# Kernel tuning notes

Hardware: AMD Instinct MI355X
Metric: run time of the kernel (lower is better)

The kernel has to match this reference:

```python
import jax, jax.numpy as jnp
import numpy as np

B, C, H, W = 4, 256, 128, 128
HEADS = 64
HD = C // HEADS  # 4
G = 32           # group norm groups
EPS = 1e-5


def setup_inputs() -> dict:
    key = jax.random.key(0)
    ks = jax.random.split(key, 6)
    x = jax.random.normal(ks[0], (B, C, H, W), dtype=jnp.float32)
    gn_weight = jnp.ones((1, C, 1, 1), dtype=jnp.float32)
    gn_bias = jnp.zeros((1, C, 1, 1), dtype=jnp.float32)
    # 1x1 convs stored as (out_ch, in_ch) matrices
    qkv_w = jax.random.normal(ks[1], (3 * C, C), dtype=jnp.float32) * 0.02
    qkv_b = jax.random.normal(ks[2], (3 * C,), dtype=jnp.float32) * 0.01
    out_w = jax.random.normal(ks[3], (C, C), dtype=jnp.float32) * 0.02
    out_b = jax.random.normal(ks[4], (C,), dtype=jnp.float32) * 0.01
    return {"x": x, "gn_weight": gn_weight, "gn_bias": gn_bias,
            "qkv_w": qkv_w, "qkv_b": qkv_b, "out_w": out_w, "out_b": out_b}


def group_norm(x, weight, bias):
    n, c, h, w = x.shape
    xg = x.reshape(n, G, -1)
    mean = xg.mean(axis=-1, keepdims=True)
    var = jnp.var(xg, axis=-1, keepdims=True, ddof=1)  # torch.var default is unbiased
    xg = (xg - mean) / jnp.sqrt(var + EPS)
    return xg.reshape(n, c, h, w) * weight + bias


def conv1x1(x, w, b):
    # x: (B, Cin, H, W), w: (Cout, Cin)
    return jnp.einsum('bchw,oc->bohw', x, w) + b[None, :, None, None]


def reference(x, gn_weight, gn_bias, qkv_w, qkv_b, out_w, out_b):
    skip = x
    h = group_norm(x, gn_weight, gn_bias)
    qkv = conv1x1(h, qkv_w, qkv_b)                      # (B, 3C, H, W)
    qkv = qkv.reshape(B, HEADS, 3 * HD, H * W)
    q, k, v = jnp.split(qkv, 3, axis=2)                  # each (B, heads, hd, HW)
    scores = jnp.einsum('bhdn,bhen->bhde', q, k) / (HD ** 0.5)  # (B, heads, hd, hd)
    scores = jax.nn.softmax(scores, axis=1)              # softmax over HEADS axis (as in source)
    out = jnp.einsum('bhde,bhen->bhdn', scores, v)       # (B, heads, hd, HW)
    out = out.reshape(B, C, H, W)
    out = conv1x1(out, out_w, out_b)
    return out + skip
```

## Files before the change

kernel.cpp:

```cpp
#include <hip/hip_runtime.h>


constexpr int kB = 4;
constexpr int kC = 256;
constexpr int kHW = 16384;
constexpr int kHeads = 64;
constexpr int kNG = 32;
constexpr int kCPG = 8;
constexpr int kCP1 = 257;
constexpr int kPS = 260;
constexpr float kEPS = 1e-5f;
constexpr int kNSplit = 32;

typedef __attribute__((ext_vector_type(8))) _Float16 f16x8;
typedef __attribute__((ext_vector_type(4))) _Float16 f16x4;
typedef __attribute__((ext_vector_type(4))) float f32x4;

union V8 { f16x8 v; uint4 u; _Float16 h[8]; };

constexpr size_t oXT    = 0;
constexpr size_t oXH    = oXT + (size_t)kB * kHW * kC / 2;
constexpr size_t oSpart = oXH + (size_t)kB * kHW * kC / 2;
constexpr size_t oS     = oSpart + (size_t)3 * kB * kNSplit * 128 * 128;
constexpr size_t oSums  = oS + (size_t)kB * kCP1 * kPS;
constexpr size_t oGv    = oSums + (size_t)kB * kC;
constexpr size_t oSc    = oGv + (size_t)kB * kC;
constexpr size_t oTc    = oSc + (size_t)kB * kC;
constexpr size_t oScore = oTc + (size_t)kB * kC;
constexpr size_t oAq    = oSpart;
constexpr size_t oM     = oXH;
constexpr size_t oGmH   = oXH + (size_t)kB * kC * kPS;

__global__ __launch_bounds__(256) void k0_tr(const float* __restrict__ x,
                                             _Float16* __restrict__ xT,
                                             _Float16* __restrict__ xH,
                                             float* __restrict__ sums) {
  const int nt = blockIdx.x, ct = blockIdx.y, b = blockIdx.z;
  __shared__ float T[64][65];
  __shared__ float psum[64][4];
  const float* xb = x + ((size_t)b * kC + ct * 64) * kHW + nt * 64;
  _Float16* xhb = xH + ((size_t)b * kC + ct * 64) * kHW + nt * 64;
  const int tid = threadIdx.x;

#pragma unroll
  for (int rep = 0; rep < 4; ++rep) {
    const int r = rep * 16 + (tid >> 4);
    const int c4 = (tid & 15) * 4;
    float4 v = *(const float4*)(xb + (size_t)r * kHW + c4);
    T[r][c4 + 0] = v.x; T[r][c4 + 1] = v.y; T[r][c4 + 2] = v.z; T[r][c4 + 3] = v.w;
    f16x4 hv = {(_Float16)v.x, (_Float16)v.y, (_Float16)v.z, (_Float16)v.w};
    *(f16x4*)(xhb + (size_t)r * kHW + c4) = hv;
  }
  __syncthreads();
  {
    const int q = tid >> 6, r = tid & 63;
    float s = 0.f;
#pragma unroll
    for (int i = 0; i < 16; ++i) s += T[r][q * 16 + i];
    psum[r][q] = s;
  }
  __syncthreads();
  if (tid < 64) {
    float s = psum[tid][0] + psum[tid][1] + psum[tid][2] + psum[tid][3];
    atomicAdd(&sums[b * kC + ct * 64 + tid], s);
  }
  const int nl = tid >> 2, cgrp = tid & 3;
  V8 lo, hi;
#pragma unroll
  for (int i = 0; i < 8; ++i)  lo.h[i] = (_Float16)T[cgrp * 16 + i][nl];
#pragma unroll
  for (int i = 0; i < 8; ++i)  hi.h[i] = (_Float16)T[cgrp * 16 + 8 + i][nl];
  _Float16* dst = xT + ((size_t)b * kHW + nt * 64 + nl) * kC + ct * 64 + cgrp * 16;
  *(uint4*)dst = lo.u;
  *(uint4*)(dst + 8) = hi.u;
}

__global__ __launch_bounds__(256) void k1_syrk(const _Float16* __restrict__ xH,
                                               float* __restrict__ Spart) {
  const int tt = blockIdx.x >> 5;
  const int sp = blockIdx.x & 31;
  const int b = blockIdx.y;
  const int ti = (tt == 2) ? 1 : 0;
  const int tj = (tt == 0) ? 0 : 1;
  const bool diag = (ti == tj);
  const _Float16* xb = xH + (size_t)b * kC * kHW;
  const int n0 = sp * (kHW / kNSplit);

  __shared__ __align__(16) _Float16 XI[128 * 64];
  __shared__ __align__(16) _Float16 XJ[128 * 64];

  const int tid = threadIdx.x;
  const int wave = tid >> 6, lane = tid & 63;
  const int wi = wave >> 1, wj = wave & 1;
  const int lrow = lane & 15, lgq = lane >> 4;

  f32x4 acc[16];
#pragma unroll
  for (int i = 0; i < 16; ++i) acc[i] = (f32x4){0.f, 0.f, 0.f, 0.f};

  for (int ch = 0; ch < kHW / kNSplit / 64; ++ch) {
    const int nb = n0 + ch * 64;
#pragma unroll
    for (int rep = 0; rep < 4; ++rep) {
      const int gi = tid + rep * 256;
      const int r = gi >> 3, g = gi & 7;
      const size_t boff = (size_t)r * 128 + (((unsigned)(g ^ (r & 7))) << 4);
      uint4 va = *(const uint4*)(xb + (size_t)(ti * 128 + r) * kHW + nb + g * 8);
      *(uint4*)((char*)XI + boff) = va;
      if (!diag) {
        uint4 vb = *(const uint4*)(xb + (size_t)(tj * 128 + r) * kHW + nb + g * 8);
        *(uint4*)((char*)XJ + boff) = vb;
      }
    }
    __syncthreads();
    const _Float16* XB = diag ? XI : XJ;
#pragma unroll
    for (int sub = 0; sub < 2; ++sub) {
      const int gq = sub * 4 + lgq;
      f16x8 afr[4], bfr[4];
#pragma unroll
      for (int ia = 0; ia < 4; ++ia) {
        const int r = wi * 64 + ia * 16 + lrow;
        afr[ia] = *(const f16x8*)((const char*)XI + (size_t)r * 128 + (((unsigned)(gq ^ (r & 7))) << 4));
      }
#pragma unroll
      for (int jb = 0; jb < 4; ++jb) {
        const int r = wj * 64 + jb * 16 + lrow;
        bfr[jb] = *(const f16x8*)((const char*)XB + (size_t)r * 128 + (((unsigned)(gq ^ (r & 7))) << 4));
      }
#pragma unroll
      for (int ia = 0; ia < 4; ++ia)
#pragma unroll
        for (int jb = 0; jb < 4; ++jb)
          acc[ia * 4 + jb] = __builtin_amdgcn_mfma_f32_16x16x32_f16(afr[ia], bfr[jb], acc[ia * 4 + jb], 0, 0, 0);
    }
    __syncthreads();
  }
  float* P = Spart + (((size_t)tt * kB + b) * kNSplit + sp) * 16384;
#pragma unroll
  for (int ia = 0; ia < 4; ++ia)
#pragma unroll
    for (int jb = 0; jb < 4; ++jb)
#pragma unroll
      for (int reg = 0; reg < 4; ++reg) {
        const int i = wi * 64 + ia * 16 + lgq * 4 + reg;
        const int j = wj * 64 + jb * 16 + lrow;
        P[(size_t)i * 128 + j] = acc[ia * 4 + jb][reg];
      }
}

__global__ __launch_bounds__(256) void k1r_reduce(const float* __restrict__ Spart,
                                                  float* __restrict__ S) {
  const int blk = blockIdx.x;
  const int tile12 = blk >> 4;
  const int part = blk & 15;
  const int tt = tile12 >> 2, b = tile12 & 3;
  const int rti = (tt == 2) ? 1 : 0;
  const int rtj = (tt == 0) ? 0 : 1;
  const int e0 = part * 1024 + threadIdx.x * 4;
  float4 s = {0.f, 0.f, 0.f, 0.f};
  const float* base = Spart + ((size_t)tt * kB + b) * kNSplit * 16384 + e0;
  for (int sp = 0; sp < kNSplit; ++sp) {
    float4 v = *(const float4*)(base + (size_t)sp * 16384);
    s.x += v.x; s.y += v.y; s.z += v.z; s.w += v.w;
  }
  const int i = e0 >> 7, j = e0 & 127;
  float* Sb = S + (size_t)b * kCP1 * kPS;
  float* dst = Sb + (size_t)(rti * 128 + i) * kPS + rtj * 128 + j;
  dst[0] = s.x; dst[1] = s.y; dst[2] = s.z; dst[3] = s.w;
  if (tt == 1) {
    Sb[(size_t)(128 + j + 0) * kPS + i] = s.x;
    Sb[(size_t)(128 + j + 1) * kPS + i] = s.y;
    Sb[(size_t)(128 + j + 2) * kPS + i] = s.z;
    Sb[(size_t)(128 + j + 3) * kPS + i] = s.w;
  }
}

__global__ __launch_bounds__(256) void k2a_stats(const float* __restrict__ S,
                                                 const float* __restrict__ sums,
                                                 const float* __restrict__ gw,
                                                 const float* __restrict__ gb,
                                                 float* __restrict__ sArr,
                                                 float* __restrict__ tArr) {
  const int b = blockIdx.x;
  const float* Sb = S + (size_t)b * kCP1 * kPS;
  __shared__ float sx[kC], sdg[kC], meanv[kNG], invv[kNG];
  const int c = threadIdx.x;
  sx[c]  = sums[b * kC + c];
  sdg[c] = Sb[(size_t)c * kPS + c];
  __syncthreads();
  if (c < kNG) {
    float sum = 0.f, ssq = 0.f;
    for (int k = 0; k < kCPG; ++k) { sum += sx[c * kCPG + k]; ssq += sdg[c * kCPG + k]; }
    const float n = (float)(kCPG * kHW);
    const float mean = sum / n;
    const float var = (ssq - n * mean * mean) / (n - 1.0f);
    meanv[c] = mean;
    invv[c] = rsqrtf(var + kEPS);
  }
  __syncthreads();
  const int g = c / kCPG;
  const float s = gw[c] * invv[g];
  sArr[b * kC + c] = s;
  tArr[b * kC + c] = gb[c] - meanv[g] * s;
}

__global__ __launch_bounds__(256) void k3a_aq(const float* __restrict__ S,
                                              const float* __restrict__ sums,
                                              const float* __restrict__ sArr,
                                              const float* __restrict__ tArr,
                                              const float* __restrict__ qkv_w,
                                              const float* __restrict__ qkv_b,
                                              float* __restrict__ Aq) {
  const int ct = blockIdx.x, mt = blockIdx.y, b = blockIdx.z;
  const float* Sb = S + (size_t)b * kCP1 * kPS;
  const float HWf = (float)kHW;
  __shared__ float Wt[32][68];
  __shared__ float Gs[32][68];
  __shared__ float shs[kC], sht[kC], shx[kC], shr[kC];
  const int tid = threadIdx.x;
  {
    const float sv = sArr[b * kC + tid];
    const float tv = tArr[b * kC + tid];
    const float xv = sums[b * kC + tid];
    shs[tid] = sv; sht[tid] = tv; shx[tid] = xv;
    shr[tid] = sv * xv + tv * HWf;
  }
  __syncthreads();
  float acc[16];
#pragma unroll
  for (int i = 0; i < 16; ++i) acc[i] = 0.f;
  const int i0 = (tid & 15) * 4;
  const int j0 = (tid >> 4) * 4;
  const int cp0 = ct * 64;

  for (int cb = 0; cb < kC; cb += 32) {
    int idx = tid;
#pragma unroll
    for (int r = 0; r < 2; ++r) {
      const int m = idx >> 3;
      const int c4 = (idx & 7) * 4;
      const int mg = mt * 64 + m;
      const int row = 12 * (mg >> 2) + (mg & 3);
      float4 v = *(const float4*)(qkv_w + (size_t)row * kC + cb + c4);
      Wt[c4 + 0][m] = v.x; Wt[c4 + 1][m] = v.y; Wt[c4 + 2][m] = v.z; Wt[c4 + 3][m] = v.w;
      idx += 256;
    }
    idx = tid;
#pragma unroll
    for (int r = 0; r < 2; ++r) {
      const int cc = idx >> 4;
      const int n4 = (idx & 15) * 4;
      const int rr = cb + cc;
      const float s_r = shs[rr], t_r = sht[rr], x_r = shx[rr];
      float4 o;
      if (cp0 + n4 < kC) {
        float4 v = *(const float4*)(Sb + (size_t)rr * kPS + cp0 + n4);
        const int cp = cp0 + n4;
        o.x = s_r * (shs[cp + 0] * v.x + sht[cp + 0] * x_r) + t_r * shr[cp + 0];
        o.y = s_r * (shs[cp + 1] * v.y + sht[cp + 1] * x_r) + t_r * shr[cp + 1];
        o.z = s_r * (shs[cp + 2] * v.z + sht[cp + 2] * x_r) + t_r * shr[cp + 2];
        o.w = s_r * (shs[cp + 3] * v.w + sht[cp + 3] * x_r) + t_r * shr[cp + 3];
      } else if (cp0 + n4 == kC) {
        o = (float4){s_r * x_r + t_r * HWf, 0.f, 0.f, 0.f};
      } else {
        o = (float4){0.f, 0.f, 0.f, 0.f};
      }
      *(float4*)&Gs[cc][n4] = o;
      idx += 256;
    }
    __syncthreads();
#pragma unroll
    for (int kk = 0; kk < 32; ++kk) {
      float4 a = *(const float4*)&Wt[kk][i0];
      float4 g = *(const float4*)&Gs[kk][j0];
      acc[0]  += a.x * g.x; acc[1]  += a.x * g.y; acc[2]  += a.x * g.z; acc[3]  += a.x * g.w;
      acc[4]  += a.y * g.x; acc[5]  += a.y * g.y; acc[6]  += a.y * g.z; acc[7]  += a.y * g.w;
      acc[8]  += a.z * g.x; acc[9]  += a.z * g.y; acc[10] += a.z * g.z; acc[11] += a.z * g.w;
      acc[12] += a.w * g.x; acc[13] += a.w * g.y; acc[14] += a.w * g.z; acc[15] += a.w * g.w;
    }
    __syncthreads();
  }
#pragma unroll
  for (int mi = 0; mi < 4; ++mi) {
    const int mg = mt * 64 + i0 + mi;
    const float bias = qkv_b[12 * (mg >> 2) + (mg & 3)];
#pragma unroll
    for (int cj = 0; cj < 4; ++cj) {
      const int cp = cp0 + j0 + cj;
      if (cp < kCP1) {
        const float g256 = (cp < kC) ? shr[cp] : HWf;
        Aq[((size_t)b * kC + mg) * kCP1 + cp] = acc[mi * 4 + cj] + bias * g256;
      }
    }
  }
}

__global__ __launch_bounds__(256) void k3b_scores(const float* __restrict__ Aq,
                                                  const float* __restrict__ qkv_w,
                                                  const float* __restrict__ qkv_b,
                                                  float* __restrict__ score) {
  const int h = blockIdx.x, b = blockIdx.y;
  const int tid = threadIdx.x, wave = tid >> 6, lane = tid & 63;
#pragma unroll
  for (int p = wave; p < 16; p += 4) {
    const int d = p >> 2, e = p & 3;
    const float* aqr = Aq + ((size_t)b * kC + h * 4 + d) * kCP1;
    const int krow = h * 12 + 4 + e;
    float s = 0.f;
#pragma unroll
    for (int it = 0; it < 4; ++it) {
      const int cp = lane + it * 64;
      s += aqr[cp] * qkv_w[(size_t)krow * kC + cp];
    }
    if (lane == 0) s += aqr[256] * qkv_b[krow];
#pragma unroll
    for (int off = 32; off; off >>= 1) s += __shfl_xor(s, off);
    if (lane == 0) score[((size_t)(b * kHeads) + h) * 16 + p] = 0.5f * s;
  }
}

__global__ __launch_bounds__(256) void k45_M(const float* __restrict__ score,
                                             const float* __restrict__ qkv_w,
                                             const float* __restrict__ qkv_b,
                                             float* __restrict__ M) {
  const int b = blockIdx.y;
  const int cidx = blockIdx.x;
  const int h = cidx >> 2, d = cidx & 3;
  __shared__ float sc[64][4];
  __shared__ float mx[4], sm[4];
  const int tid = threadIdx.x;
  {
    const int h2 = tid >> 2, e = tid & 3;
    sc[h2][e] = score[((size_t)(b * kHeads) + h2) * 16 + d * 4 + e];
  }
  __syncthreads();
  const int wave = tid >> 6, lane = tid & 63;
  {
    const float v = sc[lane][wave];
    float m = v;
#pragma unroll
    for (int off = 32; off; off >>= 1) m = fmaxf(m, __shfl_xor(m, off));
    float e2 = expf(v - m);
#pragma unroll
    for (int off = 32; off; off >>= 1) e2 += __shfl_xor(e2, off);
    if (lane == 0) { mx[wave] = m; sm[wave] = e2; }
  }
  __syncthreads();
  const float p0 = expf(sc[h][0] - mx[0]) / sm[0];
  const float p1 = expf(sc[h][1] - mx[1]) / sm[1];
  const float p2 = expf(sc[h][2] - mx[2]) / sm[2];
  const float p3 = expf(sc[h][3] - mx[3]) / sm[3];
  for (int cp = tid; cp < kCP1; cp += 256) {
    float a;
    if (cp < kC) {
      a = p0 * qkv_w[(size_t)(h * 12 + 8 + 0) * kC + cp] +
          p1 * qkv_w[(size_t)(h * 12 + 8 + 1) * kC + cp] +
          p2 * qkv_w[(size_t)(h * 12 + 8 + 2) * kC + cp] +
          p3 * qkv_w[(size_t)(h * 12 + 8 + 3) * kC + cp];
    } else {
      a = p0 * qkv_b[h * 12 + 8 + 0] + p1 * qkv_b[h * 12 + 8 + 1] +
          p2 * qkv_b[h * 12 + 8 + 2] + p3 * qkv_b[h * 12 + 8 + 3];
    }
    M[((size_t)b * kC + cidx) * kPS + cp] = a;
  }
}

__global__ __launch_bounds__(256) void k5b_gemm(const float* __restrict__ M,
                                                const float* __restrict__ out_w,
                                                const float* __restrict__ sArr,
                                                const float* __restrict__ tArr,
                                                _Float16* __restrict__ GmH,
                                                float* __restrict__ gvec) {
  const int ct = blockIdx.x, ot = blockIdx.y, b = blockIdx.z;
  const float* Mb = M + (size_t)b * kC * kPS;
  __shared__ float Wt[32][68];
  __shared__ float Gs[32][68];
  __shared__ float gred[64][17];
  float acc[16];
#pragma unroll
  for (int i = 0; i < 16; ++i) acc[i] = 0.f;
  const int tid = threadIdx.x;
  const int i0 = (tid & 15) * 4;
  const int j0 = (tid >> 4) * 4;
  const int cp0 = ct * 64;

  for (int cb = 0; cb < kC; cb += 32) {
    int idx = tid;
#pragma unroll
    for (int r = 0; r < 2; ++r) {
      const int m = idx >> 3;
      const int c4 = (idx & 7) * 4;
      float4 v = *(const float4*)(out_w + (size_t)(ot * 64 + m) * kC + cb + c4);
      Wt[c4 + 0][m] = v.x; Wt[c4 + 1][m] = v.y; Wt[c4 + 2][m] = v.z; Wt[c4 + 3][m] = v.w;
      idx += 256;
    }
    idx = tid;
#pragma unroll
    for (int r = 0; r < 2; ++r) {
      const int cc = idx >> 4;
      const int n4 = (idx & 15) * 4;
      float4 v = {0.f, 0.f, 0.f, 0.f};
      if (cp0 + n4 < kCP1) v = *(const float4*)(Mb + (size_t)(cb + cc) * kPS + cp0 + n4);
      *(float4*)&Gs[cc][n4] = v;
      idx += 256;
    }
    __syncthreads();
#pragma unroll
    for (int kk = 0; kk < 32; ++kk) {
      float4 a = *(const float4*)&Wt[kk][i0];
      float4 g = *(const float4*)&Gs[kk][j0];
      acc[0]  += a.x * g.x; acc[1]  += a.x * g.y; acc[2]  += a.x * g.z; acc[3]  += a.x * g.w;
      acc[4]  += a.y * g.x; acc[5]  += a.y * g.y; acc[6]  += a.y * g.z; acc[7]  += a.y * g.w;
      acc[8]  += a.z * g.x; acc[9]  += a.z * g.y; acc[10] += a.z * g.z; acc[11] += a.z * g.w;
      acc[12] += a.w * g.x; acc[13] += a.w * g.y; acc[14] += a.w * g.z; acc[15] += a.w * g.w;
    }
    __syncthreads();
  }
  float gpart[4] = {0.f, 0.f, 0.f, 0.f};
#pragma unroll
  for (int mi = 0; mi < 4; ++mi) {
    const int o = ot * 64 + i0 + mi;
#pragma unroll
    for (int cj = 0; cj < 4; ++cj) {
      const int cp = cp0 + j0 + cj;
      const float f = acc[mi * 4 + cj];
      if (cp < kC) {
        GmH[((size_t)b * kC + o) * kC + cp] = (_Float16)(f * sArr[b * kC + cp]);
        gpart[mi] += f * tArr[b * kC + cp];
      } else if (cp == kC) {
        gpart[mi] += f;
      }
    }
  }
#pragma unroll
  for (int mi = 0; mi < 4; ++mi) gred[i0 + mi][tid >> 4] = gpart[mi];
  __syncthreads();
  if (tid < 64) {
    float s = 0.f;
#pragma unroll
    for (int k = 0; k < 16; ++k) s += gred[tid][k];
    atomicAdd(&gvec[b * kC + ot * 64 + tid], s);
  }
}

__global__ __launch_bounds__(256) void k6_final(const _Float16* __restrict__ xT,
                                                const _Float16* __restrict__ GmH,
                                                const float* __restrict__ gvec,
                                                const float* __restrict__ out_b,
                                                const float* __restrict__ x,
                                                float* __restrict__ out) {
  const int nt = blockIdx.x, ot = blockIdx.y, b = blockIdx.z;
  __shared__ __align__(16) char smem[64 * 132 * 4];
  _Float16* GT = (_Float16*)smem;
  _Float16* XT = (_Float16*)(smem + 16384);
  float* Ep = (float*)smem;
  const int tid = threadIdx.x;
  const int wave = tid >> 6, lane = tid & 63;
  const int wo = wave >> 1, wn = wave & 1;
  const int lrow = lane & 15, lgq = lane >> 4;

  f32x4 acc[16];
#pragma unroll
  for (int i = 0; i < 16; ++i) acc[i] = (f32x4){0.f, 0.f, 0.f, 0.f};

  for (int cc = 0; cc < kC; cc += 64) {
#pragma unroll
    for (int rep = 0; rep < 4; ++rep) {
      const int gi = tid + rep * 256;
      const int r = gi >> 3, g = gi & 7;
      const size_t boff = (size_t)r * 128 + (((unsigned)(g ^ (r & 7))) << 4);
      uint4 gv = *(const uint4*)(GmH + ((size_t)(b * kC + ot * 128 + r)) * kC + cc + g * 8);
      *(uint4*)((char*)GT + boff) = gv;
      uint4 xv = *(const uint4*)(xT + ((size_t)b * kHW + nt * 128 + r) * kC + cc + g * 8);
      *(uint4*)((char*)XT + boff) = xv;
    }
    __syncthreads();
#pragma unroll
    for (int sub = 0; sub < 2; ++sub) {
      const int gq = sub * 4 + lgq;
      f16x8 afr[4], bfr[4];
#pragma unroll
      for (int ia = 0; ia < 4; ++ia) {
        const int r = wo * 64 + ia * 16 + lrow;
        afr[ia] = *(const f16x8*)((const char*)GT + (size_t)r * 128 + (((unsigned)(gq ^ (r & 7))) << 4));
      }
#pragma unroll
      for (int jb = 0; jb < 4; ++jb) {
        const int r = wn * 64 + jb * 16 + lrow;
        bfr[jb] = *(const f16x8*)((const char*)XT + (size_t)r * 128 + (((unsigned)(gq ^ (r & 7))) << 4));
      }
#pragma unroll
      for (int ia = 0; ia < 4; ++ia)
#pragma unroll
        for (int jb = 0; jb < 4; ++jb)
          acc[ia * 4 + jb] = __builtin_amdgcn_mfma_f32_16x16x32_f16(afr[ia], bfr[jb], acc[ia * 4 + jb], 0, 0, 0);
    }
    __syncthreads();
  }
#pragma unroll
  for (int p = 0; p < 2; ++p) {
    if (wo == p) {
#pragma unroll
      for (int ia = 0; ia < 4; ++ia)
#pragma unroll
        for (int jb = 0; jb < 4; ++jb)
#pragma unroll
          for (int reg = 0; reg < 4; ++reg)
            Ep[(size_t)(ia * 16 + lgq * 4 + reg) * 132 + wn * 64 + jb * 16 + lrow] =
                acc[ia * 4 + jb][reg];
    }
    __syncthreads();
#pragma unroll
    for (int it = 0; it < 8; ++it) {
      const int id = it * 256 + tid;
      const int row = id >> 5, nc = (id & 31) * 4;
      const int o = ot * 128 + p * 64 + row;
      const float gvv = gvec[b * kC + o] + out_b[o];
      float4 e = *(const float4*)&Ep[(size_t)row * 132 + nc];
      const size_t gidx = ((size_t)b * kC + o) * kHW + nt * 128 + nc;
      float4 sk = *(const float4*)&x[gidx];
      float4 res = {e.x + gvv + sk.x, e.y + gvv + sk.y, e.z + gvv + sk.z, e.w + gvv + sk.w};
      *(float4*)&out[gidx] = res;
    }
    __syncthreads();
  }
}

extern "C" void kernel_launch(void* const* d_in, const int* in_sizes, int n_in,
                              void* d_out, int out_size, void* d_ws, size_t ws_size,
                              hipStream_t stream) {
  const float* x    = (const float*)d_in[0];
  const float* gnw  = (const float*)d_in[1];
  const float* gnb  = (const float*)d_in[2];
  const float* qkvw = (const float*)d_in[3];
  const float* qkvb = (const float*)d_in[4];
  const float* outw = (const float*)d_in[5];
  const float* outb = (const float*)d_in[6];
  float* out = (float*)d_out;
  float* ws = (float*)d_ws;

  _Float16* xT   = (_Float16*)(ws + oXT);
  _Float16* xH   = (_Float16*)(ws + oXH);
  float* Spart   = ws + oSpart;
  float* S       = ws + oS;
  float* sums    = ws + oSums;
  float* gv      = ws + oGv;
  float* sArr    = ws + oSc;
  float* tArr    = ws + oTc;
  float* score   = ws + oScore;
  float* Aq      = ws + oAq;
  float* M       = ws + oM;
  _Float16* GmH  = (_Float16*)(ws + oGmH);

  hipMemsetAsync(sums, 0, (size_t)2 * kB * kC * sizeof(float), stream);
  k0_tr<<<dim3(kHW / 64, kC / 64, kB), 256, 0, stream>>>(x, xT, xH, sums);
  k1_syrk<<<dim3(3 * kNSplit, kB), 256, 0, stream>>>(xH, Spart);
  k1r_reduce<<<dim3(3 * kB * 16), 256, 0, stream>>>(Spart, S);
  k2a_stats<<<kB, 256, 0, stream>>>(S, sums, gnw, gnb, sArr, tArr);
  k3a_aq<<<dim3(5, 4, kB), 256, 0, stream>>>(S, sums, sArr, tArr, qkvw, qkvb, Aq);
  k3b_scores<<<dim3(kHeads, kB), 256, 0, stream>>>(Aq, qkvw, qkvb, score);
  k45_M<<<dim3(kC, kB), 256, 0, stream>>>(score, qkvw, qkvb, M);
  k5b_gemm<<<dim3(5, 4, kB), 256, 0, stream>>>(M, outw, sArr, tArr, GmH, gv);
  k6_final<<<dim3(kHW / 128, kC / 128, kB), 256, 0, stream>>>(xT, GmH, gv, outb, x, out);
}
```

Before: 238.9 us.

## Fold skip into GEMM identity, replace atomics with partial buffers, fuse softmax

Adds the identity to the fused output matrix so the residual skip comes from the fp16 transposed input inside the final GEMM, which removes the fp32 re-read of x in the epilogue. Replaces atomicAdd reductions and the memset with per-tile partial buffers that later kernels sum. Moves the softmax into the scores kernel so the M kernel only reads probabilities. The skip path now carries fp16 rounding of x, which is a precision risk, and the gvP sum reads only 5 of the 8 partial slots, which presumes just 5 ct tiles write them.

```diff
diff --git a/kernel.cpp b/kernel.cpp
--- a/kernel.cpp
+++ b/kernel.cpp
@@ -22,11 +22,12 @@
 constexpr size_t oXH    = oXT + (size_t)kB * kHW * kC / 2;
 constexpr size_t oSpart = oXH + (size_t)kB * kHW * kC / 2;
 constexpr size_t oS     = oSpart + (size_t)3 * kB * kNSplit * 128 * 128;
-constexpr size_t oSums  = oS + (size_t)kB * kCP1 * kPS;
-constexpr size_t oGv    = oSums + (size_t)kB * kC;
-constexpr size_t oSc    = oGv + (size_t)kB * kC;
+constexpr size_t oSumsP = oS + (size_t)kB * kCP1 * kPS;
+constexpr size_t oSums  = oSumsP + (size_t)kB * 256 * kC;
+constexpr size_t oGvP   = oSums + (size_t)kB * kC;
+constexpr size_t oSc    = oGvP + (size_t)kB * kC * 8;
 constexpr size_t oTc    = oSc + (size_t)kB * kC;
-constexpr size_t oScore = oTc + (size_t)kB * kC;
+constexpr size_t oP     = oTc + (size_t)kB * kC;
 constexpr size_t oAq    = oSpart;
 constexpr size_t oM     = oXH;
 constexpr size_t oGmH   = oXH + (size_t)kB * kC * kPS;
@@ -34,7 +35,7 @@
 __global__ __launch_bounds__(256) void k0_tr(const float* __restrict__ x,
                                              _Float16* __restrict__ xT,
                                              _Float16* __restrict__ xH,
-                                             float* __restrict__ sums) {
+                                             float* __restrict__ sumsP) {
   const int nt = blockIdx.x, ct = blockIdx.y, b = blockIdx.z;
   __shared__ float T[64][65];
   __shared__ float psum[64][4];
@@ -62,7 +63,7 @@
   __syncthreads();
   if (tid < 64) {
     float s = psum[tid][0] + psum[tid][1] + psum[tid][2] + psum[tid][3];
-    atomicAdd(&sums[b * kC + ct * 64 + tid], s);
+    sumsP[((size_t)b * 256 + nt) * kC + ct * 64 + tid] = s;
   }
   const int nl = tid >> 2, cgrp = tid & 3;
   V8 lo, hi;
@@ -177,16 +178,20 @@
 }
 
 __global__ __launch_bounds__(256) void k2a_stats(const float* __restrict__ S,
-                                                 const float* __restrict__ sums,
+                                                 const float* __restrict__ sumsP,
                                                  const float* __restrict__ gw,
                                                  const float* __restrict__ gb,
                                                  float* __restrict__ sArr,
-                                                 float* __restrict__ tArr) {
+                                                 float* __restrict__ tArr,
+                                                 float* __restrict__ sums) {
   const int b = blockIdx.x;
   const float* Sb = S + (size_t)b * kCP1 * kPS;
   __shared__ float sx[kC], sdg[kC], meanv[kNG], invv[kNG];
   const int c = threadIdx.x;
-  sx[c]  = sums[b * kC + c];
+  float accs = 0.f;
+  for (int nt = 0; nt < 256; ++nt) accs += sumsP[((size_t)b * 256 + nt) * kC + c];
+  sums[b * kC + c] = accs;
+  sx[c]  = accs;
   sdg[c] = Sb[(size_t)c * kPS + c];
   __syncthreads();
   if (c < kNG) {
@@ -296,15 +301,16 @@
   }
 }
 
-__global__ __launch_bounds__(256) void k3b_scores(const float* __restrict__ Aq,
-                                                  const float* __restrict__ qkv_w,
-                                                  const float* __restrict__ qkv_b,
-                                                  float* __restrict__ score) {
-  const int h = blockIdx.x, b = blockIdx.y;
+__global__ __launch_bounds__(256) void k3b_sm(const float* __restrict__ Aq,
+                                              const float* __restrict__ qkv_w,
+                                              const float* __restrict__ qkv_b,
+                                              float* __restrict__ P) {
+  const int de = blockIdx.x, b = blockIdx.y;
+  const int d = de >> 2, e = de & 3;
+  __shared__ float sc[64];
   const int tid = threadIdx.x, wave = tid >> 6, lane = tid & 63;
-#pragma unroll
-  for (int p = wave; p < 16; p += 4) {
-    const int d = p >> 2, e = p & 3;
+  for (int hh = 0; hh < 16; ++hh) {
+    const int h = wave * 16 + hh;
     const float* aqr = Aq + ((size_t)b * kC + h * 4 + d) * kCP1;
     const int krow = h * 12 + 4 + e;
     float s = 0.f;
@@ -316,42 +322,34 @@
     if (lane == 0) s += aqr[256] * qkv_b[krow];
 #pragma unroll
     for (int off = 32; off; off >>= 1) s += __shfl_xor(s, off);
-    if (lane == 0) score[((size_t)(b * kHeads) + h) * 16 + p] = 0.5f * s;
-  }
-}
-
-__global__ __launch_bounds__(256) void k45_M(const float* __restrict__ score,
+    if (lane == 0) sc[h] = 0.5f * s;
+  }
+  __syncthreads();
+  if (tid < 64) {
+    const float v = sc[tid];
+    float m = v;
+#pragma unroll
+    for (int off = 32; off; off >>= 1) m = fmaxf(m, __shfl_xor(m, off));
+    float ex = expf(v - m);
+    float ssum = ex;
+#pragma unroll
+    for (int off = 32; off; off >>= 1) ssum += __shfl_xor(ssum, off);
+    P[((size_t)(b * kHeads) + tid) * 16 + de] = ex / ssum;
+  }
+}
+
+__global__ __launch_bounds__(256) void k5a_M(const float* __restrict__ P,
                                              const float* __restrict__ qkv_w,
                                              const float* __restrict__ qkv_b,
                                              float* __restrict__ M) {
   const int b = blockIdx.y;
   const int cidx = blockIdx.x;
   const int h = cidx >> 2, d = cidx & 3;
-  __shared__ float sc[64][4];
-  __shared__ float mx[4], sm[4];
-  const int tid = threadIdx.x;
-  {
-    const int h2 = tid >> 2, e = tid & 3;
-    sc[h2][e] = score[((size_t)(b * kHeads) + h2) * 16 + d * 4 + e];
-  }
-  __syncthreads();
-  const int wave = tid >> 6, lane = tid & 63;
-  {
-    const float v = sc[lane][wave];
-    float m = v;
-#pragma unroll
-    for (int off = 32; off; off >>= 1) m = fmaxf(m, __shfl_xor(m, off));
-    float e2 = expf(v - m);
-#pragma unroll
-    for (int off = 32; off; off >>= 1) e2 += __shfl_xor(e2, off);
-    if (lane == 0) { mx[wave] = m; sm[wave] = e2; }
-  }
-  __syncthreads();
-  const float p0 = expf(sc[h][0] - mx[0]) / sm[0];
-  const float p1 = expf(sc[h][1] - mx[1]) / sm[1];
-  const float p2 = expf(sc[h][2] - mx[2]) / sm[2];
-  const float p3 = expf(sc[h][3] - mx[3]) / sm[3];
-  for (int cp = tid; cp < kCP1; cp += 256) {
+  const float p0 = P[((size_t)(b * kHeads) + h) * 16 + d * 4 + 0];
+  const float p1 = P[((size_t)(b * kHeads) + h) * 16 + d * 4 + 1];
+  const float p2 = P[((size_t)(b * kHeads) + h) * 16 + d * 4 + 2];
+  const float p3 = P[((size_t)(b * kHeads) + h) * 16 + d * 4 + 3];
+  for (int cp = threadIdx.x; cp < kCP1; cp += 256) {
     float a;
     if (cp < kC) {
       a = p0 * qkv_w[(size_t)(h * 12 + 8 + 0) * kC + cp] +
@@ -371,7 +369,7 @@
                                                 const float* __restrict__ sArr,
                                                 const float* __restrict__ tArr,
                                                 _Float16* __restrict__ GmH,
-                                                float* __restrict__ gvec) {
+                                                float* __restrict__ gvP) {
   const int ct = blockIdx.x, ot = blockIdx.y, b = blockIdx.z;
   const float* Mb = M + (size_t)b * kC * kPS;
   __shared__ float Wt[32][68];
@@ -426,7 +424,8 @@
       const int cp = cp0 + j0 + cj;
       const float f = acc[mi * 4 + cj];
       if (cp < kC) {
-        GmH[((size_t)b * kC + o) * kC + cp] = (_Float16)(f * sArr[b * kC + cp]);
+        const float val = f * sArr[b * kC + cp] + ((cp == o) ? 1.0f : 0.0f);
+        GmH[((size_t)b * kC + o) * kC + cp] = (_Float16)val;
         gpart[mi] += f * tArr[b * kC + cp];
       } else if (cp == kC) {
         gpart[mi] += f;
@@ -440,18 +439,18 @@
     float s = 0.f;
 #pragma unroll
     for (int k = 0; k < 16; ++k) s += gred[tid][k];
-    atomicAdd(&gvec[b * kC + ot * 64 + tid], s);
+    gvP[((size_t)b * kC + ot * 64 + tid) * 8 + ct] = s;
   }
 }
 
 __global__ __launch_bounds__(256) void k6_final(const _Float16* __restrict__ xT,
                                                 const _Float16* __restrict__ GmH,
-                                                const float* __restrict__ gvec,
+                                                const float* __restrict__ gvP,
                                                 const float* __restrict__ out_b,
-                                                const float* __restrict__ x,
                                                 float* __restrict__ out) {
   const int nt = blockIdx.x, ot = blockIdx.y, b = blockIdx.z;
   __shared__ __align__(16) char smem[64 * 132 * 4];
+  __shared__ float gvs[128];
   _Float16* GT = (_Float16*)smem;
   _Float16* XT = (_Float16*)(smem + 16384);
   float* Ep = (float*)smem;
@@ -459,6 +458,12 @@
   const int wave = tid >> 6, lane = tid & 63;
   const int wo = wave >> 1, wn = wave & 1;
   const int lrow = lane & 15, lgq = lane >> 4;
+
+  if (tid < 128) {
+    const int o = ot * 128 + tid;
+    const float* gp = gvP + ((size_t)b * kC + o) * 8;
+    gvs[tid] = gp[0] + gp[1] + gp[2] + gp[3] + gp[4] + out_b[o];
+  }
 
   f32x4 acc[16];
 #pragma unroll
@@ -516,11 +521,10 @@
       const int id = it * 256 + tid;
       const int row = id >> 5, nc = (id & 31) * 4;
       const int o = ot * 128 + p * 64 + row;
-      const float gvv = gvec[b * kC + o] + out_b[o];
+      const float gvv = gvs[p * 64 + row];
       float4 e = *(const float4*)&Ep[(size_t)row * 132 + nc];
       const size_t gidx = ((size_t)b * kC + o) * kHW + nt * 128 + nc;
-      float4 sk = *(const float4*)&x[gidx];
-      float4 res = {e.x + gvv + sk.x, e.y + gvv + sk.y, e.z + gvv + sk.z, e.w + gvv + sk.w};
+      float4 res = {e.x + gvv, e.y + gvv, e.z + gvv, e.w + gvv};
       *(float4*)&out[gidx] = res;
     }
     __syncthreads();
@@ -544,23 +548,23 @@
   _Float16* xH   = (_Float16*)(ws + oXH);
   float* Spart   = ws + oSpart;
   float* S       = ws + oS;
+  float* sumsP   = ws + oSumsP;
   float* sums    = ws + oSums;
-  float* gv      = ws + oGv;
+  float* gvP     = ws + oGvP;
   float* sArr    = ws + oSc;
   float* tArr    = ws + oTc;
-  float* score   = ws + oScore;
+  float* P       = ws + oP;
   float* Aq      = ws + oAq;
   float* M       = ws + oM;
   _Float16* GmH  = (_Float16*)(ws + oGmH);
 
-  hipMemsetAsync(sums, 0, (size_t)2 * kB * kC * sizeof(float), stream);
-  k0_tr<<<dim3(kHW / 64, kC / 64, kB), 256, 0, stream>>>(x, xT, xH, sums);
+  k0_tr<<<dim3(kHW / 64, kC / 64, kB), 256, 0, stream>>>(x, xT, xH, sumsP);
   k1_syrk<<<dim3(3 * kNSplit, kB), 256, 0, stream>>>(xH, Spart);
   k1r_reduce<<<dim3(3 * kB * 16), 256, 0, stream>>>(Spart, S);
-  k2a_stats<<<kB, 256, 0, stream>>>(S, sums, gnw, gnb, sArr, tArr);
+  k2a_stats<<<kB, 256, 0, stream>>>(S, sumsP, gnw, gnb, sArr, tArr, sums);
   k3a_aq<<<dim3(5, 4, kB), 256, 0, stream>>>(S, sums, sArr, tArr, qkvw, qkvb, Aq);
-  k3b_scores<<<dim3(kHeads, kB), 256, 0, stream>>>(Aq, qkvw, qkvb, score);
-  k45_M<<<dim3(kC, kB), 256, 0, stream>>>(score, qkvw, qkvb, M);
-  k5b_gemm<<<dim3(5, 4, kB), 256, 0, stream>>>(M, outw, sArr, tArr, GmH, gv);
-  k6_final<<<dim3(kHW / 128, kC / 128, kB), 256, 0, stream>>>(xT, GmH, gv, outb, x, out);
-}
+  k3b_sm<<<dim3(16, kB), 256, 0, stream>>>(Aq, qkvw, qkvb, P);
+  k5a_M<<<dim3(kC, kB), 256, 0, stream>>>(P, qkvw, qkvb, M);
+  k5b_gemm<<<dim3(5, 4, kB), 256, 0, stream>>>(M, outw, sArr, tArr, GmH, gvP);
+  k6_final<<<dim3(kHW / 128, kC / 128, kB), 256, 0, stream>>>(xT, GmH, gvP, outb, out);
+}
```

New measurement: 239.3 us. About the same (+0.2%).
